# Optimization experiments

Measured on AMD Instinct MI355X. Metric: run time of the kernel, lower is better.

## Reference

```python
import jax, jax.numpy as jnp
import numpy as np

T, H, I, E, K = 1024, 2048, 1408, 8, 2  # tokens, hidden, moe_intermediate, n_experts, top_k

def setup_inputs() -> dict:
    key = jax.random.key(0)
    k0, k1, k2, k3 = jax.random.split(key, 4)
    def w(k, shape, fan_in):
        return jax.random.normal(k, shape, jnp.float32) / np.float32(np.sqrt(fan_in))
    return {
        "hidden_states": jax.random.normal(k0, (T, H), jnp.float32),
        "gate_w": w(k1, (H, E), H),      # router: LiteLinear(H -> E), no bias
        "w1": w(k2, (E, H, I), H),        # experts_w1 [E, H, I]
        "w2": w(k3, (E, I, H), I),        # experts_w2 [E, I, H]
    }

def reference(hidden_states, gate_w, w1, w2):
    # Router: logits -> softmax -> top-k expert probabilities (no renorm; Qwen2MoE norm_topk_prob=False)
    router_logits = hidden_states @ gate_w                      # [T, E]
    probs = jax.nn.softmax(router_logits, axis=-1)              # [T, E]
    topk_vals, topk_idx = jax.lax.top_k(probs, K)               # [T, K]
    # Dense combine weights: zero except at the top-k experts of each token
    combine = jnp.sum(jax.nn.one_hot(topk_idx, E, dtype=probs.dtype) * topk_vals[..., None], axis=1)  # [T, E]
    # Expert MLP per source: down(silu(x @ w1)) — note: no gate/up split in this repo's fused_moe weights
    h = jnp.einsum('th,ehi->tei', hidden_states, w1)            # [T, E, I]
    y = jnp.einsum('tei,eih->teh', jax.nn.silu(h), w2)          # [T, E, H]
    return jnp.einsum('te,teh->th', combine, y)                 # [T, H]
```

## Files before the change

### kernel.cpp

```cpp
#include <hip/hip_runtime.h>
#include <hip/hip_fp16.h>

#define T_TOK 1024
#define H_DIM 2048
#define I_DIM 1408
#define N_EXP 8
#define TOPK  2

using f16x8 = __attribute__((ext_vector_type(8))) _Float16;
using f32x4 = __attribute__((ext_vector_type(4))) float;

#define BM 128
#define BN 64
#define BK 64
#define NTHR 512

#define BAR()                                                     \
    do {                                                          \
        asm volatile("s_waitcnt lgkmcnt(0)" ::: "memory");        \
        __builtin_amdgcn_s_barrier();                             \
    } while (0)

#define WS_COUNTS      0
#define WS_BASES       256
#define WS_CURSORS     512
#define WS_TOPK_E      768
#define WS_TOPK_W      (768 + 8192)
#define WS_TOK_OF_SLOT 17408
#define WS_W_OF_SLOT   29696
#define WS_HACT        43008
#define WS_NEEDED      (43008 + 8650752)

__global__ void k_router(const float* __restrict__ X, const float* __restrict__ GW,
                         int* __restrict__ counts, int* __restrict__ topk_e,
                         float* __restrict__ topk_w) {
    int t = (blockIdx.x * blockDim.x + threadIdx.x) >> 6;
    int lane = threadIdx.x & 63;
    if (t >= T_TOK) return;
    float acc[N_EXP];
#pragma unroll
    for (int e = 0; e < N_EXP; ++e) acc[e] = 0.f;
    const float* xrow = X + (size_t)t * H_DIM;
    for (int h = lane; h < H_DIM; h += 64) {
        float x = xrow[h];
        const float* g = GW + (size_t)h * N_EXP;
#pragma unroll
        for (int e = 0; e < N_EXP; ++e) acc[e] = fmaf(x, g[e], acc[e]);
    }
#pragma unroll
    for (int off = 32; off > 0; off >>= 1) {
#pragma unroll
        for (int e = 0; e < N_EXP; ++e) acc[e] += __shfl_xor(acc[e], off, 64);
    }
    if (lane == 0) {
        float m = acc[0];
#pragma unroll
        for (int e = 1; e < N_EXP; ++e) m = fmaxf(m, acc[e]);
        float ex[N_EXP], s = 0.f;
#pragma unroll
        for (int e = 0; e < N_EXP; ++e) { ex[e] = expf(acc[e] - m); s += ex[e]; }
        float inv = 1.f / s;
        int e1 = 0;
#pragma unroll
        for (int e = 1; e < N_EXP; ++e) if (ex[e] > ex[e1]) e1 = e;
        int e2 = (e1 == 0) ? 1 : 0;
#pragma unroll
        for (int e = 0; e < N_EXP; ++e) if (e != e1 && ex[e] > ex[e2]) e2 = e;
        topk_e[t * 2 + 0] = e1;
        topk_e[t * 2 + 1] = e2;
        topk_w[t * 2 + 0] = ex[e1] * inv;
        topk_w[t * 2 + 1] = ex[e2] * inv;
        atomicAdd(&counts[e1], 1);
        atomicAdd(&counts[e2], 1);
    }
}

__global__ void k_prefix(const int* __restrict__ counts, int* __restrict__ bases,
                         int* __restrict__ cursors) {
    if (threadIdx.x == 0) {
        int b = 0;
        for (int e = 0; e < N_EXP; ++e) {
            bases[e] = b;
            b += ((counts[e] + BM - 1) / BM) * BM;
            cursors[e] = 0;
        }
    }
}

__global__ void k_scatter(const int* __restrict__ topk_e, const float* __restrict__ topk_w,
                          const int* __restrict__ bases, int* __restrict__ cursors,
                          int* __restrict__ tok_of_slot, float* __restrict__ w_of_slot) {
    int t = blockIdx.x * blockDim.x + threadIdx.x;
    if (t >= T_TOK) return;
    for (int j = 0; j < TOPK; ++j) {
        int e = topk_e[t * 2 + j];
        int pos = atomicAdd(&cursors[e], 1);
        int slot = bases[e] + pos;
        tok_of_slot[slot] = t;
        w_of_slot[slot] = topk_w[t * 2 + j];
    }
}


#define G_COMPUTE(buf)                                                          \
    do {                                                                        \
        _Pragma("unroll") for (int ks = 0; ks < 2; ++ks) {                      \
            f16x8 af[2], bf[2];                                                 \
            _Pragma("unroll") for (int ii = 0; ii < 2; ++ii) {                  \
                int r = wm + ii * 16 + rsel;                                    \
                af[ii] = *(const f16x8*)&As[buf][r][((kq + 4 * ks) ^ (r & 7)) * 8]; \
            }                                                                   \
            _Pragma("unroll") for (int jj = 0; jj < 2; ++jj) {                  \
                int r = wn + jj * 16 + rsel;                                    \
                bf[jj] = *(const f16x8*)&Bs[buf][r][((kq + 4 * ks) ^ (r & 7)) * 8]; \
            }                                                                   \
            _Pragma("unroll") for (int ii = 0; ii < 2; ++ii)                    \
                _Pragma("unroll") for (int jj = 0; jj < 2; ++jj)                \
                    acc[ii][jj] = __builtin_amdgcn_mfma_f32_16x16x32_f16(af[ii], bf[jj], acc[ii][jj], 0, 0, 0); \
        }                                                                       \
    } while (0)

__global__ __launch_bounds__(NTHR, 4) void k_gemm1(
    const float* __restrict__ X, const float* __restrict__ W1,
    const int* __restrict__ counts, const int* __restrict__ bases,
    const int* __restrict__ tok_of_slot, const float* __restrict__ w_of_slot,
    _Float16* __restrict__ hact) {
    __shared__ _Float16 As[2][BM][BK];
    __shared__ _Float16 Bs[2][BN][BK];

    const int e = blockIdx.z;
    const int cnt = counts[e];
    const int m0 = blockIdx.y * BM;
    if (m0 >= cnt) return;
    const int base = bases[e];
    const int n0 = blockIdx.x * BN;
    const int tid = threadIdx.x;

    const int ar = tid >> 2;
    const int ac2 = (tid & 3) * 2;
    const int r_eff = min(ar, cnt - m0 - 1);
    const float* arow = X + (size_t)tok_of_slot[base + m0 + r_eff] * H_DIM + (tid & 3) * 16;

    const int bn = tid & 63;
    const int bc = tid >> 6;
    const float* bcol = W1 + (size_t)e * (H_DIM * I_DIM) + (size_t)(bc * 8) * I_DIM + n0 + bn;

    const int wid = tid >> 6, lane = tid & 63;
    const int wm = (wid >> 1) * 32, wn = (wid & 1) * 32;
    const int rsel = lane & 15, kq = lane >> 4;

    f32x4 acc[2][2] = {};

    float4 aR0[4]; float bR0[8];
    float4 aR1[4]; float bR1[8];

#define LOAD1(aR, bR, k0)                                              \
    do {                                                               \
        aR[0] = *(const float4*)(arow + (k0));                         \
        aR[1] = *(const float4*)(arow + (k0) + 4);                     \
        aR[2] = *(const float4*)(arow + (k0) + 8);                     \
        aR[3] = *(const float4*)(arow + (k0) + 12);                    \
        const float* bp = bcol + (size_t)(k0) * I_DIM;                 \
        _Pragma("unroll") for (int j = 0; j < 8; ++j)                  \
            bR[j] = bp[(size_t)j * I_DIM];                             \
    } while (0)

#define STORE1(buf, aR, bR)                                            \
    do {                                                               \
        f16x8 p0, p1;                                                  \
        _Pragma("unroll") for (int j = 0; j < 4; ++j) {                \
            p0[j]     = (_Float16)aR[0][j];                            \
            p0[j + 4] = (_Float16)aR[1][j];                            \
            p1[j]     = (_Float16)aR[2][j];                            \
            p1[j + 4] = (_Float16)aR[3][j];                            \
        }                                                              \
        *(f16x8*)&As[buf][ar][((ac2) ^ (ar & 7)) * 8] = p0;            \
        *(f16x8*)&As[buf][ar][((ac2 + 1) ^ (ar & 7)) * 8] = p1;        \
        f16x8 q;                                                       \
        _Pragma("unroll") for (int j = 0; j < 8; ++j)                  \
            q[j] = (_Float16)bR[j];                                    \
        *(f16x8*)&Bs[buf][bn][(bc ^ (bn & 7)) * 8] = q;                \
    } while (0)

    const int KT = H_DIM / BK;
    LOAD1(aR0, bR0, 0);
    STORE1(0, aR0, bR0);
    LOAD1(aR0, bR0, BK);
    BAR();
    for (int kt = 0; kt < KT; kt += 2) {
        if (kt + 2 < KT) LOAD1(aR1, bR1, (kt + 2) * BK);
        G_COMPUTE(0);
        if (kt + 1 < KT) STORE1(1, aR0, bR0);
        BAR();
        if (kt + 3 < KT) LOAD1(aR0, bR0, (kt + 3) * BK);
        if (kt + 1 < KT) {
            G_COMPUTE(1);
            if (kt + 2 < KT) STORE1(0, aR1, bR1);
            BAR();
        }
    }
#undef LOAD1
#undef STORE1

    const int rows = cnt - m0;
#pragma unroll
    for (int i = 0; i < 2; ++i) {
#pragma unroll
        for (int rg = 0; rg < 4; ++rg) {
            int r = wm + i * 16 + kq * 4 + rg;
            if (r < rows) {
                int slot = base + m0 + r;
                float w = w_of_slot[slot];
                _Float16* hrow = hact + (size_t)slot * I_DIM + n0;
#pragma unroll
                for (int j = 0; j < 2; ++j) {
                    float v = acc[i][j][rg];
                    hrow[wn + j * 16 + rsel] = (_Float16)(v / (1.f + expf(-v)) * w);
                }
            }
        }
    }
}

__global__ __launch_bounds__(NTHR, 4) void k_gemm2(
    const _Float16* __restrict__ hact, const float* __restrict__ W2,
    const int* __restrict__ counts, const int* __restrict__ bases,
    const int* __restrict__ tok_of_slot, float* __restrict__ out) {
    __shared__ _Float16 As[2][BM][BK];
    __shared__ _Float16 Bs[2][BN][BK];

    const int e = blockIdx.z;
    const int cnt = counts[e];
    const int m0 = blockIdx.y * BM;
    if (m0 >= cnt) return;
    const int base = bases[e];
    const int n0 = blockIdx.x * BN;
    const int tid = threadIdx.x;

    const int ar = tid >> 2;
    const int ac2 = (tid & 3) * 2;
    const int r_eff = min(ar, cnt - m0 - 1);
    const _Float16* arow = hact + (size_t)(base + m0 + r_eff) * I_DIM + (tid & 3) * 16;

    const int bn = tid & 63;
    const int bc = tid >> 6;
    const float* bcol = W2 + (size_t)e * (I_DIM * H_DIM) + (size_t)(bc * 8) * H_DIM + n0 + bn;

    const int wid = tid >> 6, lane = tid & 63;
    const int wm = (wid >> 1) * 32, wn = (wid & 1) * 32;
    const int rsel = lane & 15, kq = lane >> 4;

    f32x4 acc[2][2] = {};

    f16x8 aR0[2]; float bR0[8];
    f16x8 aR1[2]; float bR1[8];

#define LOAD2(aR, bR, k0)                                              \
    do {                                                               \
        aR[0] = *(const f16x8*)(arow + (k0));                          \
        aR[1] = *(const f16x8*)(arow + (k0) + 8);                      \
        const float* bp = bcol + (size_t)(k0) * H_DIM;                 \
        _Pragma("unroll") for (int j = 0; j < 8; ++j)                  \
            bR[j] = bp[(size_t)j * H_DIM];                             \
    } while (0)

#define STORE2(buf, aR, bR)                                            \
    do {                                                               \
        *(f16x8*)&As[buf][ar][((ac2) ^ (ar & 7)) * 8] = aR[0];         \
        *(f16x8*)&As[buf][ar][((ac2 + 1) ^ (ar & 7)) * 8] = aR[1];     \
        f16x8 q;                                                       \
        _Pragma("unroll") for (int j = 0; j < 8; ++j)                  \
            q[j] = (_Float16)bR[j];                                    \
        *(f16x8*)&Bs[buf][bn][(bc ^ (bn & 7)) * 8] = q;                \
    } while (0)

    const int KT = I_DIM / BK;
    LOAD2(aR0, bR0, 0);
    STORE2(0, aR0, bR0);
    LOAD2(aR0, bR0, BK);
    BAR();
    for (int kt = 0; kt < KT; kt += 2) {
        if (kt + 2 < KT) LOAD2(aR1, bR1, (kt + 2) * BK);
        G_COMPUTE(0);
        if (kt + 1 < KT) STORE2(1, aR0, bR0);
        BAR();
        if (kt + 3 < KT) LOAD2(aR0, bR0, (kt + 3) * BK);
        if (kt + 1 < KT) {
            G_COMPUTE(1);
            if (kt + 2 < KT) STORE2(0, aR1, bR1);
            BAR();
        }
    }
#undef LOAD2
#undef STORE2

    const int rows = cnt - m0;
#pragma unroll
    for (int i = 0; i < 2; ++i) {
#pragma unroll
        for (int rg = 0; rg < 4; ++rg) {
            int r = wm + i * 16 + kq * 4 + rg;
            if (r < rows) {
                int slot = base + m0 + r;
                int tok = tok_of_slot[slot];
                float* orow = out + (size_t)tok * H_DIM + n0;
#pragma unroll
                for (int j = 0; j < 2; ++j)
                    atomicAdd(&orow[wn + j * 16 + rsel], acc[i][j][rg]);
            }
        }
    }
}

extern "C" void kernel_launch(void* const* d_in, const int* in_sizes, int n_in,
                              void* d_out, int out_size, void* d_ws, size_t ws_size,
                              hipStream_t stream) {
    const float* X  = (const float*)d_in[0];
    const float* GW = (const float*)d_in[1];
    const float* W1 = (const float*)d_in[2];
    const float* W2 = (const float*)d_in[3];
    float* out = (float*)d_out;
    char* ws = (char*)d_ws;
    if (ws_size < (size_t)WS_NEEDED) return;

    int*   counts      = (int*)(ws + WS_COUNTS);
    int*   bases       = (int*)(ws + WS_BASES);
    int*   cursors     = (int*)(ws + WS_CURSORS);
    int*   topk_e      = (int*)(ws + WS_TOPK_E);
    float* topk_w      = (float*)(ws + WS_TOPK_W);
    int*   tok_of_slot = (int*)(ws + WS_TOK_OF_SLOT);
    float* w_of_slot   = (float*)(ws + WS_W_OF_SLOT);
    _Float16* hact     = (_Float16*)(ws + WS_HACT);

    hipMemsetAsync(counts, 0, N_EXP * sizeof(int), stream);
    hipMemsetAsync(out, 0, (size_t)T_TOK * H_DIM * sizeof(float), stream);
    k_router<<<T_TOK / 4, 256, 0, stream>>>(X, GW, counts, topk_e, topk_w);
    k_prefix<<<1, 64, 0, stream>>>(counts, bases, cursors);
    k_scatter<<<T_TOK / 256, 256, 0, stream>>>(topk_e, topk_w, bases, cursors,
                                               tok_of_slot, w_of_slot);
    k_gemm1<<<dim3(I_DIM / BN, T_TOK / BM, N_EXP), NTHR, 0, stream>>>(
        X, W1, counts, bases, tok_of_slot, w_of_slot, hact);
    k_gemm2<<<dim3(H_DIM / BN, T_TOK / BM, N_EXP), NTHR, 0, stream>>>(
        hact, W2, counts, bases, tok_of_slot, out);
}
```

Before: 167.8 us.

## Split-K gemm1 with fp32 atomics, move SiLU into gemm2, drop prefix kernel

The first expert GEMM is split into two K halves, doubling the block count, and each half accumulates into an fp32 intermediate buffer with atomics. SiLU and the routing weight move into gemm2's A-tile load path. The prefix kernel is removed, and each kernel recomputes expert bases from the counts. The output zeroing moves into the router kernel. This trades extra atomics, a larger fp32 intermediate with its own memset, and redundant expf work in gemm2 for more parallelism and fewer launches.

```diff
diff --git a/kernel.cpp b/kernel.cpp
--- a/kernel.cpp
+++ b/kernel.cpp
@@ -22,19 +22,33 @@
     } while (0)
 
 #define WS_COUNTS      0
-#define WS_BASES       256
 #define WS_CURSORS     512
 #define WS_TOPK_E      768
 #define WS_TOPK_W      (768 + 8192)
 #define WS_TOK_OF_SLOT 17408
 #define WS_W_OF_SLOT   29696
-#define WS_HACT        43008
-#define WS_NEEDED      (43008 + 8650752)
+#define WS_H32         43008
+#define WS_NEEDED      (43008 + 17301504)
+
+__device__ __forceinline__ void prefix_of(const int* counts, int e, int& base, int& cnt) {
+    int b = 0;
+#pragma unroll
+    for (int q = 0; q < N_EXP; ++q) {
+        int c = counts[q];
+        if (q == e) { base = b; cnt = c; }
+        b += ((c + BM - 1) / BM) * BM;
+    }
+}
 
 __global__ void k_router(const float* __restrict__ X, const float* __restrict__ GW,
                          int* __restrict__ counts, int* __restrict__ topk_e,
-                         float* __restrict__ topk_w) {
-    int t = (blockIdx.x * blockDim.x + threadIdx.x) >> 6;
+                         float* __restrict__ topk_w, float* __restrict__ out) {
+    int gtid = blockIdx.x * blockDim.x + threadIdx.x;
+    float4* o4 = (float4*)out;
+    for (int i = gtid; i < T_TOK * H_DIM / 4; i += (T_TOK / 4) * 256)
+        o4[i] = float4{0.f, 0.f, 0.f, 0.f};
+
+    int t = gtid >> 6;
     int lane = threadIdx.x & 63;
     if (t >= T_TOK) return;
     float acc[N_EXP];
@@ -75,27 +89,17 @@
     }
 }
 
-__global__ void k_prefix(const int* __restrict__ counts, int* __restrict__ bases,
-                         int* __restrict__ cursors) {
-    if (threadIdx.x == 0) {
-        int b = 0;
-        for (int e = 0; e < N_EXP; ++e) {
-            bases[e] = b;
-            b += ((counts[e] + BM - 1) / BM) * BM;
-            cursors[e] = 0;
-        }
-    }
-}
-
 __global__ void k_scatter(const int* __restrict__ topk_e, const float* __restrict__ topk_w,
-                          const int* __restrict__ bases, int* __restrict__ cursors,
+                          const int* __restrict__ counts, int* __restrict__ cursors,
                           int* __restrict__ tok_of_slot, float* __restrict__ w_of_slot) {
     int t = blockIdx.x * blockDim.x + threadIdx.x;
     if (t >= T_TOK) return;
     for (int j = 0; j < TOPK; ++j) {
         int e = topk_e[t * 2 + j];
+        int base, cnt;
+        prefix_of(counts, e, base, cnt);
         int pos = atomicAdd(&cursors[e], 1);
-        int slot = bases[e] + pos;
+        int slot = base + pos;
         tok_of_slot[slot] = t;
         w_of_slot[slot] = topk_w[t * 2 + j];
     }
@@ -122,28 +126,31 @@
 
 __global__ __launch_bounds__(NTHR, 4) void k_gemm1(
     const float* __restrict__ X, const float* __restrict__ W1,
-    const int* __restrict__ counts, const int* __restrict__ bases,
-    const int* __restrict__ tok_of_slot, const float* __restrict__ w_of_slot,
-    _Float16* __restrict__ hact) {
+    const int* __restrict__ counts, const int* __restrict__ tok_of_slot,
+    float* __restrict__ h32) {
     __shared__ _Float16 As[2][BM][BK];
     __shared__ _Float16 Bs[2][BN][BK];
 
     const int e = blockIdx.z;
-    const int cnt = counts[e];
-    const int m0 = blockIdx.y * BM;
+    int base, cnt;
+    prefix_of(counts, e, base, cnt);
+    const int mblk = blockIdx.y & 7;
+    const int kh = blockIdx.y >> 3;
+    const int m0 = mblk * BM;
     if (m0 >= cnt) return;
-    const int base = bases[e];
     const int n0 = blockIdx.x * BN;
     const int tid = threadIdx.x;
 
     const int ar = tid >> 2;
     const int ac2 = (tid & 3) * 2;
     const int r_eff = min(ar, cnt - m0 - 1);
-    const float* arow = X + (size_t)tok_of_slot[base + m0 + r_eff] * H_DIM + (tid & 3) * 16;
+    const float* arow = X + (size_t)tok_of_slot[base + m0 + r_eff] * H_DIM
+                          + kh * 1024 + (tid & 3) * 16;
 
     const int bn = tid & 63;
     const int bc = tid >> 6;
-    const float* bcol = W1 + (size_t)e * (H_DIM * I_DIM) + (size_t)(bc * 8) * I_DIM + n0 + bn;
+    const float* bcol = W1 + (size_t)e * (H_DIM * I_DIM)
+                           + (size_t)(kh * 1024 + bc * 8) * I_DIM + n0 + bn;
 
     const int wid = tid >> 6, lane = tid & 63;
     const int wm = (wid >> 1) * 32, wn = (wid & 1) * 32;
@@ -182,7 +189,7 @@
         *(f16x8*)&Bs[buf][bn][(bc ^ (bn & 7)) * 8] = q;                \
     } while (0)
 
-    const int KT = H_DIM / BK;
+    const int KT = 1024 / BK;
     LOAD1(aR0, bR0, 0);
     STORE1(0, aR0, bR0);
     LOAD1(aR0, bR0, BK);
@@ -210,37 +217,35 @@
             int r = wm + i * 16 + kq * 4 + rg;
             if (r < rows) {
                 int slot = base + m0 + r;
-                float w = w_of_slot[slot];
-                _Float16* hrow = hact + (size_t)slot * I_DIM + n0;
-#pragma unroll
-                for (int j = 0; j < 2; ++j) {
-                    float v = acc[i][j][rg];
-                    hrow[wn + j * 16 + rsel] = (_Float16)(v / (1.f + expf(-v)) * w);
-                }
+                float* hrow = h32 + (size_t)slot * I_DIM + n0;
+#pragma unroll
+                for (int j = 0; j < 2; ++j)
+                    atomicAdd(&hrow[wn + j * 16 + rsel], acc[i][j][rg]);
             }
         }
     }
 }
 
 __global__ __launch_bounds__(NTHR, 4) void k_gemm2(
-    const _Float16* __restrict__ hact, const float* __restrict__ W2,
-    const int* __restrict__ counts, const int* __restrict__ bases,
-    const int* __restrict__ tok_of_slot, float* __restrict__ out) {
+    const float* __restrict__ h32, const float* __restrict__ W2,
+    const int* __restrict__ counts, const int* __restrict__ tok_of_slot,
+    const float* __restrict__ w_of_slot, float* __restrict__ out) {
     __shared__ _Float16 As[2][BM][BK];
     __shared__ _Float16 Bs[2][BN][BK];
 
     const int e = blockIdx.z;
-    const int cnt = counts[e];
+    int base, cnt;
+    prefix_of(counts, e, base, cnt);
     const int m0 = blockIdx.y * BM;
     if (m0 >= cnt) return;
-    const int base = bases[e];
     const int n0 = blockIdx.x * BN;
     const int tid = threadIdx.x;
 
     const int ar = tid >> 2;
     const int ac2 = (tid & 3) * 2;
     const int r_eff = min(ar, cnt - m0 - 1);
-    const _Float16* arow = hact + (size_t)(base + m0 + r_eff) * I_DIM + (tid & 3) * 16;
+    const float* arow = h32 + (size_t)(base + m0 + r_eff) * I_DIM + (tid & 3) * 16;
+    const float w_a = w_of_slot[base + m0 + r_eff];
 
     const int bn = tid & 63;
     const int bc = tid >> 6;
@@ -252,13 +257,15 @@
 
     f32x4 acc[2][2] = {};
 
-    f16x8 aR0[2]; float bR0[8];
-    f16x8 aR1[2]; float bR1[8];
+    float4 aR0[4]; float bR0[8];
+    float4 aR1[4]; float bR1[8];
 
 #define LOAD2(aR, bR, k0)                                              \
     do {                                                               \
-        aR[0] = *(const f16x8*)(arow + (k0));                          \
-        aR[1] = *(const f16x8*)(arow + (k0) + 8);                      \
+        aR[0] = *(const float4*)(arow + (k0));                         \
+        aR[1] = *(const float4*)(arow + (k0) + 4);                     \
+        aR[2] = *(const float4*)(arow + (k0) + 8);                     \
+        aR[3] = *(const float4*)(arow + (k0) + 12);                    \
         const float* bp = bcol + (size_t)(k0) * H_DIM;                 \
         _Pragma("unroll") for (int j = 0; j < 8; ++j)                  \
             bR[j] = bp[(size_t)j * H_DIM];                             \
@@ -266,8 +273,17 @@
 
 #define STORE2(buf, aR, bR)                                            \
     do {                                                               \
-        *(f16x8*)&As[buf][ar][((ac2) ^ (ar & 7)) * 8] = aR[0];         \
-        *(f16x8*)&As[buf][ar][((ac2 + 1) ^ (ar & 7)) * 8] = aR[1];     \
+        f16x8 p0, p1;                                                  \
+        _Pragma("unroll") for (int j = 0; j < 4; ++j) {                \
+            float v00 = aR[0][j], v01 = aR[1][j];                      \
+            float v10 = aR[2][j], v11 = aR[3][j];                      \
+            p0[j]     = (_Float16)(v00 / (1.f + expf(-v00)) * w_a);    \
+            p0[j + 4] = (_Float16)(v01 / (1.f + expf(-v01)) * w_a);    \
+            p1[j]     = (_Float16)(v10 / (1.f + expf(-v10)) * w_a);    \
+            p1[j + 4] = (_Float16)(v11 / (1.f + expf(-v11)) * w_a);    \
+        }                                                              \
+        *(f16x8*)&As[buf][ar][((ac2) ^ (ar & 7)) * 8] = p0;            \
+        *(f16x8*)&As[buf][ar][((ac2 + 1) ^ (ar & 7)) * 8] = p1;        \
         f16x8 q;                                                       \
         _Pragma("unroll") for (int j = 0; j < 8; ++j)                  \
             q[j] = (_Float16)bR[j];                                    \
@@ -324,22 +340,20 @@
     if (ws_size < (size_t)WS_NEEDED) return;
 
     int*   counts      = (int*)(ws + WS_COUNTS);
-    int*   bases       = (int*)(ws + WS_BASES);
     int*   cursors     = (int*)(ws + WS_CURSORS);
     int*   topk_e      = (int*)(ws + WS_TOPK_E);
     float* topk_w      = (float*)(ws + WS_TOPK_W);
     int*   tok_of_slot = (int*)(ws + WS_TOK_OF_SLOT);
     float* w_of_slot   = (float*)(ws + WS_W_OF_SLOT);
-    _Float16* hact     = (_Float16*)(ws + WS_HACT);
-
-    hipMemsetAsync(counts, 0, N_EXP * sizeof(int), stream);
-    hipMemsetAsync(out, 0, (size_t)T_TOK * H_DIM * sizeof(float), stream);
-    k_router<<<T_TOK / 4, 256, 0, stream>>>(X, GW, counts, topk_e, topk_w);
-    k_prefix<<<1, 64, 0, stream>>>(counts, bases, cursors);
-    k_scatter<<<T_TOK / 256, 256, 0, stream>>>(topk_e, topk_w, bases, cursors,
+    float* h32         = (float*)(ws + WS_H32);
+
+    hipMemsetAsync(ws, 0, 768, stream);
+    hipMemsetAsync(h32, 0, (size_t)3072 * I_DIM * sizeof(float), stream);
+    k_router<<<T_TOK / 4, 256, 0, stream>>>(X, GW, counts, topk_e, topk_w, out);
+    k_scatter<<<T_TOK / 256, 256, 0, stream>>>(topk_e, topk_w, counts, cursors,
                                                tok_of_slot, w_of_slot);
-    k_gemm1<<<dim3(I_DIM / BN, T_TOK / BM, N_EXP), NTHR, 0, stream>>>(
-        X, W1, counts, bases, tok_of_slot, w_of_slot, hact);
-    k_gemm2<<<dim3(H_DIM / BN, T_TOK / BM, N_EXP), NTHR, 0, stream>>>(
-        hact, W2, counts, bases, tok_of_slot, out);
-}
+    k_gemm1<<<dim3(I_DIM / BN, 16, N_EXP), NTHR, 0, stream>>>(
+        X, W1, counts, tok_of_slot, h32);
+    k_gemm2<<<dim3(H_DIM / BN, 8, N_EXP), NTHR, 0, stream>>>(
+        h32, W2, counts, tok_of_slot, w_of_slot, out);
+}
```

New measurement: 250.7 us. +49.4%, slower.
